# Optimization experiments

Hardware: AMD Instinct MI355X
Metric: run time of the kernel (lower is better)

## Reference

```python
import jax, jax.numpy as jnp
import numpy as np

B, R, D, H, C = 256, 100, 6168, 128, 100  # batch, replicas, in_dim, hidden, classes


def setup_inputs() -> dict:
    key = jax.random.key(0)
    k1, k2, k3, k4, k5, k6 = jax.random.split(key, 6)
    # binary input features (texas dataset is binary; original casts to bool)
    x = jax.random.randint(k1, (B, D), 0, 2).astype(jnp.int32)
    # Bernoulli(0.5) flip mask, one per replica per feature
    noise = jax.random.randint(k2, (B, R, D), 0, 2).astype(jnp.int32)
    s1 = 1.0 / np.sqrt(D)
    W1 = jax.random.uniform(k3, (D, H), minval=-s1, maxval=s1, dtype=jnp.float32)
    b1 = jax.random.uniform(k4, (H,), minval=-s1, maxval=s1, dtype=jnp.float32)
    s2 = 1.0 / np.sqrt(H)
    W2 = jax.random.uniform(k5, (H, C), minval=-s2, maxval=s2, dtype=jnp.float32)
    b2 = jax.random.uniform(k6, (C,), minval=-s2, maxval=s2, dtype=jnp.float32)
    return {"x": x, "noise": noise, "W1": W1, "b1": b1, "W2": W2, "b2": b2}


def reference(x, noise, W1, b1, W2, b2):
    # np.invert(x, where=noise) on booleans == flip bit where noise==1
    xb = x[:, None, :]                                   # [B,1,D]
    x_noisy = jnp.where(noise == 1, 1 - xb, xb).astype(W1.dtype)  # [B,R,D]
    h = jnp.tanh(jnp.einsum('brd,dh->brh', x_noisy, W1) + b1)      # [B,R,H]
    logits = jnp.einsum('brh,hc->brc', h, W2) + b2                 # [B,R,C]
    return logits.mean(axis=1)                                     # [B,C]
```

## Files before the change

kernel.cpp:

```cpp
#include <hip/hip_runtime.h>
#include <hip/hip_bf16.h>

#define NB 256
#define NR 100
#define ND 6168
#define DP 6272
#define NH 128
#define NC 100
#define NSEG 98
#define ABUF 32768
#define ROWB 24672
#define W1T_BYTES ((size_t)NH * DP * 2)

typedef __attribute__((ext_vector_type(8))) __bf16 bf16x8;
typedef __attribute__((ext_vector_type(4))) float f32x4;
typedef __attribute__((ext_vector_type(4))) int i32x4;
typedef __attribute__((ext_vector_type(4))) unsigned int u32x4;
typedef unsigned int u32;

typedef const __attribute__((address_space(1))) u32* gas_ptr;
typedef __attribute__((address_space(3))) u32* las_ptr;

__device__ __forceinline__ void gload16(const void* g, void* l) {
  __builtin_amdgcn_global_load_lds((gas_ptr)g, (las_ptr)l, 16, 0, 0);
}

#define SB() __builtin_amdgcn_sched_barrier(0)
#define VBAR16() do { SB(); asm volatile("s_waitcnt vmcnt(16)"); SB(); \
  asm volatile("s_waitcnt lgkmcnt(0)"); SB(); __builtin_amdgcn_s_barrier(); SB(); } while (0)

__global__ void prep_w1t(const float* __restrict__ W1, __hip_bfloat16* __restrict__ W1T) {
  __shared__ float tile[32][NH + 1];
  const int d0 = blockIdx.x * 32;
  const int t = threadIdx.x;
#pragma unroll
  for (int p = 0; p < 16; ++p) {
    int idx = p * 256 + t;
    int dd = idx >> 7;
    int h  = idx & 127;
    int d  = d0 + dd;
    tile[dd][h] = (d < ND) ? W1[d * NH + h] : 0.f;
  }
  __syncthreads();
#pragma unroll
  for (int p = 0; p < 16; ++p) {
    int idx = p * 256 + t;
    int h  = idx >> 5;
    int dd = idx & 31;
    W1T[h * DP + d0 + dd] = __float2bfloat16(tile[dd][h]);
  }
}

__launch_bounds__(512, 2)
__global__ void fused_main(const int* __restrict__ x,
                           const int* __restrict__ noise,
                           const __hip_bfloat16* __restrict__ W1T,
                           const float* __restrict__ b1,
                           const float* __restrict__ W2,
                           const float* __restrict__ b2,
                           float* __restrict__ out) {
  __shared__ __align__(16) char lds[12544 + 4 * ABUF];
  u32* xpair = (u32*)lds;
  char* const Ab = lds + 12544;

  const int tid  = threadIdx.x;
  const int lane = tid & 63;
  const int w    = tid >> 6;
  const int wm   = w >> 2;
  const int wn   = w & 3;
  const int lq   = lane >> 4;
  const int lm   = lane & 15;
  const int b    = blockIdx.x;

  const char* nsrc[4];
  u32 offmax[4];
  int dofs[4];
  {
    const size_t nb = (size_t)b * NR * ND;
#pragma unroll
    for (int i = 0; i < 4; ++i) {
      int c   = w * 4 + i;
      int row = c * 4 + (lane >> 4);
      int gr  = (row < NR) ? row : (NR - 1);
      int sg  = (lane & 15) ^ (row & 7);
      nsrc[i]   = (const char*)(noise + nb + (size_t)gr * ND) + sg * 16;
      offmax[i] = (u32)(ROWB - 16 - sg * 16);
      dofs[i]   = c * 1024;
    }
  }
  const __hip_bfloat16* wsrc0 = W1T + (size_t)(wn * 32 + lm) * DP + lq * 8;
  const __hip_bfloat16* wsrc1 = W1T + (size_t)(wn * 32 + 16 + lm) * DP + lq * 8;

  f32x4 acc[4][2] = {};
  struct Bregs { bf16x8 f[4]; };
  Bregs Bcur, Bnxt;

  auto STAGE = [&](int ss, int bufidx) {
    char* dstb = Ab + bufidx * ABUF;
    const u32 off = (u32)(ss * 256);
#pragma unroll
    for (int i = 0; i < 4; ++i) {
      u32 o = (off > offmax[i]) ? offmax[i] : off;
      gload16(nsrc[i] + o, dstb + dofs[i]);
    }
  };

  auto BLOAD = [&](int s, Bregs& Br) {
#pragma unroll
    for (int kt = 0; kt < 2; ++kt) {
      Br.f[kt * 2 + 0] = *(const bf16x8*)(wsrc0 + s * 64 + kt * 32);
      Br.f[kt * 2 + 1] = *(const bf16x8*)(wsrc1 + s * 64 + kt * 32);
    }
  };

  auto COMPUTE = [&](int s, const char* A, const Bregs& Br) {
#pragma unroll
    for (int kt = 0; kt < 2; ++kt) {
      u32x4 xp = *(const u32x4*)(xpair + s * 32 + kt * 16 + lq * 4);
#pragma unroll
      for (int mf = 0; mf < 4; ++mf) {
        const int row  = wm * 64 + mf * 16 + lm;
        const int off0 = row * 256 + (((kt * 8 + lq * 2) ^ (row & 7)) * 16);
        i32x4 v0 = *(const i32x4*)(A + off0);
        i32x4 v1 = *(const i32x4*)(A + (off0 ^ 16));
        u32 q0 = (((u32)v0[0] | ((u32)v0[1] << 16)) ^ xp[0]) * 0x3F80u;
        u32 q1 = (((u32)v0[2] | ((u32)v0[3] << 16)) ^ xp[1]) * 0x3F80u;
        u32 q2 = (((u32)v1[0] | ((u32)v1[1] << 16)) ^ xp[2]) * 0x3F80u;
        u32 q3 = (((u32)v1[2] | ((u32)v1[3] << 16)) ^ xp[3]) * 0x3F80u;
        u32x4 pkv = {q0, q1, q2, q3};
        bf16x8 af = *(bf16x8*)&pkv;
        acc[mf][0] = __builtin_amdgcn_mfma_f32_16x16x32_bf16(af, Br.f[kt * 2 + 0], acc[mf][0], 0, 0, 0);
        acc[mf][1] = __builtin_amdgcn_mfma_f32_16x16x32_bf16(af, Br.f[kt * 2 + 1], acc[mf][1], 0, 0, 0);
      }
    }
  };

  STAGE(0, 0);
  STAGE(1, 1);
  STAGE(2, 2);
  BLOAD(0, Bcur);
  {
    const int* xb = x + b * ND;
    for (int i = tid; i < DP / 2; i += 512) {
      u32 p = 0;
      if (2 * i + 1 < ND) {
        int2 v = *(const int2*)(xb + 2 * i);
        p = ((u32)v.x & 1u) | (((u32)v.y & 1u) << 16);
      }
      xpair[i] = p;
    }
  }
  __syncthreads();

#pragma unroll 1
  for (int s = 0; s < NSEG; s += 2) {
    {
      VBAR16();
      int sn = (s + 1 < NSEG) ? (s + 1) : (NSEG - 1);
      BLOAD(sn, Bnxt);
      SB();
      int sc = (s + 3 < NSEG) ? (s + 3) : (NSEG - 1);
      STAGE(sc, (s + 3) & 3);
      SB();
      COMPUTE(s, Ab + (s & 3) * ABUF, Bcur);
    }
    {
      VBAR16();
      int sn = (s + 2 < NSEG) ? (s + 2) : (NSEG - 1);
      BLOAD(sn, Bcur);
      SB();
      int sc = (s + 4 < NSEG) ? (s + 4) : (NSEG - 1);
      STAGE(sc, (s + 4) & 3);
      SB();
      COMPUTE(s + 1, Ab + ((s + 1) & 3) * ABUF, Bnxt);
    }
  }

  __syncthreads();
  float* hpart = (float*)lds;
  float* hbar  = (float*)(lds + 1024);
#pragma unroll
  for (int nf = 0; nf < 2; ++nf) {
    int hcol = wn * 32 + nf * 16 + lm;
    float bb = b1[hcol];
    float ssum = 0.f;
#pragma unroll
    for (int mf = 0; mf < 4; ++mf) {
#pragma unroll
      for (int rg = 0; rg < 4; ++rg) {
        int m = wm * 64 + mf * 16 + lq * 4 + rg;
        float tv = tanhf(acc[mf][nf][rg] + bb);
        ssum += (m < NR) ? tv : 0.f;
      }
    }
    ssum += __shfl_xor(ssum, 16, 64);
    ssum += __shfl_xor(ssum, 32, 64);
    if (lq == 0) hpart[wm * 128 + hcol] = ssum;
  }
  __syncthreads();
  if (tid < NH) hbar[tid] = (hpart[tid] + hpart[128 + tid]) * (1.0f / NR);
  __syncthreads();
  if (tid < NC) {
    float sacc = b2[tid];
#pragma unroll 8
    for (int h = 0; h < NH; ++h) sacc += hbar[h] * W2[h * NC + tid];
    out[b * NC + tid] = sacc;
  }
}

extern "C" void kernel_launch(void* const* d_in, const int* in_sizes, int n_in,
                              void* d_out, int out_size, void* d_ws, size_t ws_size,
                              hipStream_t stream) {
  (void)in_sizes; (void)n_in; (void)out_size; (void)ws_size;
  const int* x     = (const int*)d_in[0];
  const int* noise = (const int*)d_in[1];
  const float* W1  = (const float*)d_in[2];
  const float* b1  = (const float*)d_in[3];
  const float* W2  = (const float*)d_in[4];
  const float* b2  = (const float*)d_in[5];
  float* out = (float*)d_out;

  __hip_bfloat16* W1T = (__hip_bfloat16*)d_ws;

  prep_w1t<<<DP / 32, 256, 0, stream>>>(W1, W1T);
  fused_main<<<NB, 512, 0, stream>>>(x, noise, W1T, b1, W2, b2, out);
}
```

Baseline: 211.7 us.

## Split noise bit-packing into a pre-pass and run GEMM on packed bits

Adds two pre-kernels. One packs x into bitmasks; the other streams the int32 noise tensor, packs it into 32-bit bitmasks and XORs them with the x bits. The GEMM kernel then loads one batch's compact bit matrix into LDS, stages W1T tiles through LDS, and expands bits to bf16 operands for MFMA. The aim is to decouple the large bandwidth-bound noise read from the MFMA pipeline and shrink the data the GEMM must consume. In exchange it adds kernel launches and a workspace round-trip, and the pack kernel's strided 16-byte loads may not coalesce well.

Result: slower. 320.2 us (+51.2%).

```diff
diff --git a/kernel.cpp b/kernel.cpp
--- a/kernel.cpp
+++ b/kernel.cpp
@@ -7,10 +7,15 @@
 #define DP 6272
 #define NH 128
 #define NC 100
-#define NSEG 98
-#define ABUF 32768
-#define ROWB 24672
+#define NW 196
+#define NWR 193
+#define ROWW 196
+#define BITS_B (NR * ROWW * 4)
 #define W1T_BYTES ((size_t)NH * DP * 2)
+#define XBITS_BYTES ((size_t)NB * ROWW * 4)
+
+#define L_B   78848
+#define L_TOT (78848 + 4 * 8192)
 
 typedef __attribute__((ext_vector_type(8))) __bf16 bf16x8;
 typedef __attribute__((ext_vector_type(4))) float f32x4;
@@ -26,7 +31,7 @@
 }
 
 #define SB() __builtin_amdgcn_sched_barrier(0)
-#define VBAR16() do { SB(); asm volatile("s_waitcnt vmcnt(16)"); SB(); \
+#define VBAR(N) do { SB(); asm volatile("s_waitcnt vmcnt(" #N ")"); SB(); \
   asm volatile("s_waitcnt lgkmcnt(0)"); SB(); __builtin_amdgcn_s_barrier(); SB(); } while (0)
 
 __global__ void prep_w1t(const float* __restrict__ W1, __hip_bfloat16* __restrict__ W1T) {
@@ -51,144 +56,114 @@
   }
 }
 
-__launch_bounds__(512, 2)
-__global__ void fused_main(const int* __restrict__ x,
-                           const int* __restrict__ noise,
-                           const __hip_bfloat16* __restrict__ W1T,
-                           const float* __restrict__ b1,
-                           const float* __restrict__ W2,
-                           const float* __restrict__ b2,
-                           float* __restrict__ out) {
-  __shared__ __align__(16) char lds[12544 + 4 * ABUF];
-  u32* xpair = (u32*)lds;
-  char* const Ab = lds + 12544;
-
+__global__ void prep_xbits(const int* __restrict__ x, u32* __restrict__ xbits) {
+  const int b = blockIdx.x, t = threadIdx.x;
+  if (t >= NWR) return;
+  const int* xp = x + (size_t)b * ND + t * 32;
+  u32 wv = 0;
+#pragma unroll
+  for (int j = 0; j < 8; ++j) {
+    if (t * 32 + j * 4 + 4 <= ND) {
+      i32x4 v = *(const i32x4*)(xp + j * 4);
+      wv |= ((u32)(v[0] & 1) << (4 * j))     | ((u32)(v[1] & 1) << (4 * j + 1))
+          | ((u32)(v[2] & 1) << (4 * j + 2)) | ((u32)(v[3] & 1) << (4 * j + 3));
+    }
+  }
+  xbits[(size_t)b * ROWW + t] = wv;
+}
+
+__global__ void pack_noise(const int* __restrict__ noise, const u32* __restrict__ xbits,
+                           u32* __restrict__ bits) {
+  const int r = blockIdx.x, b = blockIdx.y, t = threadIdx.x;
+  if (t >= NWR) return;
+  const int* np = noise + ((size_t)b * NR + r) * ND + t * 32;
+  u32 wv = 0;
+#pragma unroll
+  for (int j = 0; j < 8; ++j) {
+    if (t * 32 + j * 4 + 4 <= ND) {
+      i32x4 v = *(const i32x4*)(np + j * 4);
+      wv |= ((u32)(v[0] & 1) << (4 * j))     | ((u32)(v[1] & 1) << (4 * j + 1))
+          | ((u32)(v[2] & 1) << (4 * j + 2)) | ((u32)(v[3] & 1) << (4 * j + 3));
+    }
+  }
+  bits[((size_t)b * NR + r) * ROWW + t] = wv ^ xbits[(size_t)b * ROWW + t];
+}
+
+__launch_bounds__(512, 1)
+__global__ void gemm(const u32* __restrict__ bits, const __hip_bfloat16* __restrict__ W1T,
+                     const float* __restrict__ b1, const float* __restrict__ W2,
+                     const float* __restrict__ b2, float* __restrict__ out) {
+  __shared__ __align__(16) char lds[L_TOT];
   const int tid  = threadIdx.x;
   const int lane = tid & 63;
   const int w    = tid >> 6;
-  const int wm   = w >> 2;
-  const int wn   = w & 3;
+  const int wm   = w >> 1;
+  const int wn   = w & 1;
   const int lq   = lane >> 4;
   const int lm   = lane & 15;
   const int b    = blockIdx.x;
 
-  const char* nsrc[4];
-  u32 offmax[4];
-  int dofs[4];
+  const char* const bsrc0 = (const char*)W1T + (size_t)(16 * w + (lane >> 2)) * (DP * 2)
+                            + (lane & 3) * 16;
+  auto BSTAGE = [&](int t) {
+    gload16(bsrc0 + t * 64, lds + L_B + (t & 3) * 8192 + w * 1024);
+  };
+
   {
-    const size_t nb = (size_t)b * NR * ND;
-#pragma unroll
-    for (int i = 0; i < 4; ++i) {
-      int c   = w * 4 + i;
-      int row = c * 4 + (lane >> 4);
-      int gr  = (row < NR) ? row : (NR - 1);
-      int sg  = (lane & 15) ^ (row & 7);
-      nsrc[i]   = (const char*)(noise + nb + (size_t)gr * ND) + sg * 16;
-      offmax[i] = (u32)(ROWB - 16 - sg * 16);
-      dofs[i]   = c * 1024;
-    }
-  }
-  const __hip_bfloat16* wsrc0 = W1T + (size_t)(wn * 32 + lm) * DP + lq * 8;
-  const __hip_bfloat16* wsrc1 = W1T + (size_t)(wn * 32 + 16 + lm) * DP + lq * 8;
-
-  f32x4 acc[4][2] = {};
-  struct Bregs { bf16x8 f[4]; };
-  Bregs Bcur, Bnxt;
-
-  auto STAGE = [&](int ss, int bufidx) {
-    char* dstb = Ab + bufidx * ABUF;
-    const u32 off = (u32)(ss * 256);
-#pragma unroll
-    for (int i = 0; i < 4; ++i) {
-      u32 o = (off > offmax[i]) ? offmax[i] : off;
-      gload16(nsrc[i] + o, dstb + dofs[i]);
-    }
-  };
-
-  auto BLOAD = [&](int s, Bregs& Br) {
-#pragma unroll
-    for (int kt = 0; kt < 2; ++kt) {
-      Br.f[kt * 2 + 0] = *(const bf16x8*)(wsrc0 + s * 64 + kt * 32);
-      Br.f[kt * 2 + 1] = *(const bf16x8*)(wsrc1 + s * 64 + kt * 32);
-    }
-  };
-
-  auto COMPUTE = [&](int s, const char* A, const Bregs& Br) {
-#pragma unroll
-    for (int kt = 0; kt < 2; ++kt) {
-      u32x4 xp = *(const u32x4*)(xpair + s * 32 + kt * 16 + lq * 4);
-#pragma unroll
-      for (int mf = 0; mf < 4; ++mf) {
-        const int row  = wm * 64 + mf * 16 + lm;
-        const int off0 = row * 256 + (((kt * 8 + lq * 2) ^ (row & 7)) * 16);
-        i32x4 v0 = *(const i32x4*)(A + off0);
-        i32x4 v1 = *(const i32x4*)(A + (off0 ^ 16));
-        u32 q0 = (((u32)v0[0] | ((u32)v0[1] << 16)) ^ xp[0]) * 0x3F80u;
-        u32 q1 = (((u32)v0[2] | ((u32)v0[3] << 16)) ^ xp[1]) * 0x3F80u;
-        u32 q2 = (((u32)v1[0] | ((u32)v1[1] << 16)) ^ xp[2]) * 0x3F80u;
-        u32 q3 = (((u32)v1[2] | ((u32)v1[3] << 16)) ^ xp[3]) * 0x3F80u;
-        u32x4 pkv = {q0, q1, q2, q3};
-        bf16x8 af = *(bf16x8*)&pkv;
-        acc[mf][0] = __builtin_amdgcn_mfma_f32_16x16x32_bf16(af, Br.f[kt * 2 + 0], acc[mf][0], 0, 0, 0);
-        acc[mf][1] = __builtin_amdgcn_mfma_f32_16x16x32_bf16(af, Br.f[kt * 2 + 1], acc[mf][1], 0, 0, 0);
-      }
-    }
-  };
-
-  STAGE(0, 0);
-  STAGE(1, 1);
-  STAGE(2, 2);
-  BLOAD(0, Bcur);
-  {
-    const int* xb = x + b * ND;
-    for (int i = tid; i < DP / 2; i += 512) {
-      u32 p = 0;
-      if (2 * i + 1 < ND) {
-        int2 v = *(const int2*)(xb + 2 * i);
-        p = ((u32)v.x & 1u) | (((u32)v.y & 1u) << 16);
-      }
-      xpair[i] = p;
-    }
-  }
-  __syncthreads();
+    const char* bb = (const char*)bits + (size_t)b * BITS_B;
+    for (int c = w; c < 77; c += 8) {
+      u32 off = (u32)(c * 1024 + lane * 16);
+      if (off > BITS_B - 16) off = BITS_B - 16;
+      gload16(bb + off, lds + c * 1024);
+    }
+  }
+  BSTAGE(0); BSTAGE(1); BSTAGE(2);
+  __syncthreads();
+
+  f32x4 acc[2][4] = {};
+  const int rb0 = (wm * 32 + lm) * 784;
+  const int rb1 = (wm * 32 + 16 + lm) * 784;
+  const int lsh = lq * 8;
 
 #pragma unroll 1
-  for (int s = 0; s < NSEG; s += 2) {
-    {
-      VBAR16();
-      int sn = (s + 1 < NSEG) ? (s + 1) : (NSEG - 1);
-      BLOAD(sn, Bnxt);
-      SB();
-      int sc = (s + 3 < NSEG) ? (s + 3) : (NSEG - 1);
-      STAGE(sc, (s + 3) & 3);
-      SB();
-      COMPUTE(s, Ab + (s & 3) * ABUF, Bcur);
-    }
-    {
-      VBAR16();
-      int sn = (s + 2 < NSEG) ? (s + 2) : (NSEG - 1);
-      BLOAD(sn, Bcur);
-      SB();
-      int sc = (s + 4 < NSEG) ? (s + 4) : (NSEG - 1);
-      STAGE(sc, (s + 4) & 3);
-      SB();
-      COMPUTE(s + 1, Ab + ((s + 1) & 3) * ABUF, Bnxt);
+  for (int t = 0; t < NW; ++t) {
+    VBAR(2);
+    if (t + 3 < NW) BSTAGE(t + 3);
+    const char* Bb = lds + L_B + (t & 3) * 8192;
+    bf16x8 bf0 = *(const bf16x8*)(Bb + (wn * 64 + lm) * 64 + lq * 16);
+    bf16x8 bf1 = *(const bf16x8*)(Bb + (wn * 64 + 16 + lm) * 64 + lq * 16);
+    bf16x8 bf2 = *(const bf16x8*)(Bb + (wn * 64 + 32 + lm) * 64 + lq * 16);
+    bf16x8 bf3 = *(const bf16x8*)(Bb + (wn * 64 + 48 + lm) * 64 + lq * 16);
+#pragma unroll
+    for (int mf = 0; mf < 2; ++mf) {
+      u32 word = *(const u32*)(lds + (mf ? rb1 : rb0) + t * 4);
+      u32 by = (word >> lsh) & 0xffu;
+      u32 p0 = ((by & 1u)  ? 0x3F80u : 0u) | ((by & 2u)   ? 0x3F800000u : 0u);
+      u32 p1 = ((by & 4u)  ? 0x3F80u : 0u) | ((by & 8u)   ? 0x3F800000u : 0u);
+      u32 p2 = ((by & 16u) ? 0x3F80u : 0u) | ((by & 32u)  ? 0x3F800000u : 0u);
+      u32 p3 = ((by & 64u) ? 0x3F80u : 0u) | ((by & 128u) ? 0x3F800000u : 0u);
+      u32x4 pk = {p0, p1, p2, p3};
+      bf16x8 af = *(bf16x8*)&pk;
+      acc[mf][0] = __builtin_amdgcn_mfma_f32_16x16x32_bf16(af, bf0, acc[mf][0], 0, 0, 0);
+      acc[mf][1] = __builtin_amdgcn_mfma_f32_16x16x32_bf16(af, bf1, acc[mf][1], 0, 0, 0);
+      acc[mf][2] = __builtin_amdgcn_mfma_f32_16x16x32_bf16(af, bf2, acc[mf][2], 0, 0, 0);
+      acc[mf][3] = __builtin_amdgcn_mfma_f32_16x16x32_bf16(af, bf3, acc[mf][3], 0, 0, 0);
     }
   }
 
   __syncthreads();
   float* hpart = (float*)lds;
-  float* hbar  = (float*)(lds + 1024);
-#pragma unroll
-  for (int nf = 0; nf < 2; ++nf) {
-    int hcol = wn * 32 + nf * 16 + lm;
-    float bb = b1[hcol];
+  float* hbar  = (float*)(lds + 2048);
+#pragma unroll
+  for (int nf = 0; nf < 4; ++nf) {
+    const int hcol = wn * 64 + nf * 16 + lm;
+    const float bb = b1[hcol];
     float ssum = 0.f;
 #pragma unroll
-    for (int mf = 0; mf < 4; ++mf) {
+    for (int mf = 0; mf < 2; ++mf) {
 #pragma unroll
       for (int rg = 0; rg < 4; ++rg) {
-        int m = wm * 64 + mf * 16 + lq * 4 + rg;
+        int m = wm * 32 + mf * 16 + lq * 4 + rg;
         float tv = tanhf(acc[mf][nf][rg] + bb);
         ssum += (m < NR) ? tv : 0.f;
       }
@@ -198,7 +173,8 @@
     if (lq == 0) hpart[wm * 128 + hcol] = ssum;
   }
   __syncthreads();
-  if (tid < NH) hbar[tid] = (hpart[tid] + hpart[128 + tid]) * (1.0f / NR);
+  if (tid < NH)
+    hbar[tid] = (hpart[tid] + hpart[128 + tid] + hpart[256 + tid] + hpart[384 + tid]) * (1.0f / NR);
   __syncthreads();
   if (tid < NC) {
     float sacc = b2[tid];
@@ -221,7 +197,11 @@
   float* out = (float*)d_out;
 
   __hip_bfloat16* W1T = (__hip_bfloat16*)d_ws;
+  u32* xbits = (u32*)((char*)d_ws + W1T_BYTES);
+  u32* bits  = (u32*)((char*)d_ws + W1T_BYTES + XBITS_BYTES);
 
   prep_w1t<<<DP / 32, 256, 0, stream>>>(W1, W1T);
-  fused_main<<<NB, 512, 0, stream>>>(x, noise, W1T, b1, W2, b2, out);
-}
+  prep_xbits<<<NB, 256, 0, stream>>>(x, xbits);
+  pack_noise<<<dim3(NR, NB), 256, 0, stream>>>(noise, xbits, bits);
+  gemm<<<NB, 512, 0, stream>>>(bits, W1T, b1, W2, b2, out);
+}
```
